# Kernel tuning notes

Measured on AMD Instinct MI355X. Metric: run time of the kernel, lower is better.

Reference implementation:

```python
import jax, jax.numpy as jnp
import numpy as np

N_NODES = 50000
N_EDGES = 500000
NODE_DIM = 128
EDGE_DIM = 64
OUT_DIM = 128


def setup_inputs() -> dict:
    key = jax.random.key(0)
    k1, k2, k3, k4, k5, k6 = jax.random.split(key, 6)
    node_feats = jax.random.normal(k1, (N_NODES, NODE_DIM), dtype=jnp.float32)
    edge_feats = jax.random.normal(k2, (N_EDGES, EDGE_DIM), dtype=jnp.float32)
    src_idx = jax.random.randint(k3, (N_EDGES,), 0, N_NODES, dtype=jnp.int32)
    dst_idx = jax.random.randint(k4, (N_EDGES,), 0, N_NODES, dtype=jnp.int32)
    in_dim = 2 * NODE_DIM + EDGE_DIM
    # nn.Linear-style init scale
    scale = 1.0 / np.sqrt(in_dim)
    W = jax.random.normal(k5, (in_dim, OUT_DIM), dtype=jnp.float32) * scale
    b = jax.random.normal(k6, (OUT_DIM,), dtype=jnp.float32) * scale
    return {"node_feats": node_feats, "edge_feats": edge_feats,
            "src_idx": src_idx, "dst_idx": dst_idx, "W": W, "b": b}


def reference(node_feats, edge_feats, src_idx, dst_idx, W, b):
    # Gather per-edge src/dst node features, concat with edge feats (residual=True)
    src = node_feats[src_idx]            # [E, node_dim]
    dst = node_feats[dst_idx]            # [E, node_dim]
    combined = jnp.concatenate([src, dst, edge_feats], axis=-1)  # [E, 2*nd+ed]
    score = combined @ W + b             # [E, out_dim]
    return score
```

## Files before the change

### kernel.cpp

```cpp
#include <hip/hip_runtime.h>
#include <hip/hip_bf16.h>
#include <cstdint>

#define N_NODES 50000
#define N_EDGES 500000
#define ND 128
#define ED 64
#define OD 128

typedef __attribute__((ext_vector_type(8))) short short8;
typedef __attribute__((ext_vector_type(4))) float f32x4;

__device__ __forceinline__ unsigned short f2bf(float f) {
    union { float f; unsigned u; } c; c.f = f;
    unsigned u = c.u;
    unsigned r = (u + 0x7FFFu + ((u >> 16) & 1u)) >> 16;
    return (unsigned short)r;
}
__device__ __forceinline__ float bf2f(unsigned short s) {
    union { unsigned u; float f; } c; c.u = ((unsigned)s) << 16;
    return c.f;
}

__global__ void prep_kernel(const float* __restrict__ W,
                            unsigned short* __restrict__ wbtNP,
                            unsigned short* __restrict__ wbtE) {
    int g = blockIdx.x * 256 + threadIdx.x;
    if (g < 256 * 128) {
        int n = g >> 7, k = g & 127;
        float v = (n < 128) ? W[k * OD + n] : W[(128 + k) * OD + (n - 128)];
        wbtNP[n * 128 + k] = f2bf(v);
    } else {
        int h = g - 256 * 128;
        int n = h >> 6, k = h & 63;
        wbtE[n * 64 + k] = f2bf(W[(256 + k) * OD + n]);
    }
}

__launch_bounds__(512)
__global__ void nodeproj_kernel(const float* __restrict__ nf,
                                const unsigned short* __restrict__ wbtNP,
                                unsigned short* __restrict__ P) {
    __shared__ char lds[16384 + 65536];
    int tid = threadIdx.x;
    int m0 = blockIdx.x * 64;

    for (int i = 0; i < 4; ++i) {
        int idx = tid + i * 512;
        int row = idx >> 5, c4 = idx & 31;
        int m = m0 + row;
        float4 v = make_float4(0.f, 0.f, 0.f, 0.f);
        if (m < N_NODES) v = *(const float4*)(nf + m * ND + c4 * 4);
        uint2 pk;
        pk.x = (unsigned)f2bf(v.x) | ((unsigned)f2bf(v.y) << 16);
        pk.y = (unsigned)f2bf(v.z) | ((unsigned)f2bf(v.w) << 16);
        int byte = (row * 256 + c4 * 8) ^ ((row & 7) << 4);
        *(uint2*)(lds + byte) = pk;
    }
    {
        const uint2* wsrc = (const uint2*)wbtNP;
        for (int i = 0; i < 16; ++i) {
            int idx = tid + i * 512;
            int row = idx >> 5, c4 = idx & 31;
            uint2 v = wsrc[row * 32 + c4];
            int byte = 16384 + ((row * 256 + c4 * 8) ^ ((row & 7) << 4));
            *(uint2*)(lds + byte) = v;
        }
    }
    __syncthreads();

    int lane = tid & 63, wid = tid >> 6;
    int wm = wid >> 1;
    int wn = wid & 1;
    f32x4 acc[8];
#pragma unroll
    for (int i = 0; i < 8; ++i) acc[i] = (f32x4){0.f, 0.f, 0.f, 0.f};

    int arow = 16 * wm + (lane & 15);
    int abase = arow * 256;
    int aswz = (arow & 7) << 4;
#pragma unroll
    for (int kc = 0; kc < 4; ++kc) {
        int kb = kc * 64 + ((lane >> 4) << 4);
        short8 a = *(const short8*)(lds + ((abase + kb) ^ aswz));
#pragma unroll
        for (int nt = 0; nt < 8; ++nt) {
            int brow = 128 * wn + 16 * nt + (lane & 15);
            short8 b = *(const short8*)(lds + 16384 + ((brow * 256 + kb) ^ ((brow & 7) << 4)));
            acc[nt] = __builtin_amdgcn_mfma_f32_16x16x32_bf16(a, b, acc[nt], 0, 0, 0);
        }
    }

    int mbase = m0 + 16 * wm + ((lane >> 4) << 2);
    int colbase = 128 * wn + (lane & 15);
#pragma unroll
    for (int nt = 0; nt < 8; ++nt) {
#pragma unroll
        for (int r = 0; r < 4; ++r) {
            int mm = mbase + r;
            if (mm < N_NODES) P[mm * 256 + colbase + 16 * nt] = f2bf(acc[nt][r]);
        }
    }
}

__launch_bounds__(256)
__global__ void edge_kernel(const float* __restrict__ ef,
                            const int* __restrict__ src,
                            const int* __restrict__ dst,
                            const unsigned short* __restrict__ wbtE,
                            const unsigned short* __restrict__ P,
                            const float* __restrict__ bias,
                            float* __restrict__ out) {
    __shared__ char lds[8192 + 16384 + 32768];
    int tid = threadIdx.x;
    int e0 = blockIdx.x * 64;

    for (int i = 0; i < 4; ++i) {
        int idx = tid + i * 256;
        int row = idx >> 4, c4 = idx & 15;
        int e = e0 + row;
        float4 v = make_float4(0.f, 0.f, 0.f, 0.f);
        if (e < N_EDGES) v = *(const float4*)(ef + e * ED + c4 * 4);
        uint2 pk;
        pk.x = (unsigned)f2bf(v.x) | ((unsigned)f2bf(v.y) << 16);
        pk.y = (unsigned)f2bf(v.z) | ((unsigned)f2bf(v.w) << 16);
        int byte = (row * 128 + c4 * 8) ^ ((row & 7) << 4);
        *(uint2*)(lds + byte) = pk;
    }
    {
        const uint2* wsrc = (const uint2*)wbtE;
        for (int i = 0; i < 8; ++i) {
            int idx = tid + i * 256;
            int row = idx >> 4, c4 = idx & 15;
            uint2 v = wsrc[row * 16 + c4];
            int byte = 8192 + ((row * 128 + c4 * 8) ^ ((row & 7) << 4));
            *(uint2*)(lds + byte) = v;
        }
    }
    __syncthreads();

    int lane = tid & 63, wid = tid >> 6;
    f32x4 acc[8];
#pragma unroll
    for (int i = 0; i < 8; ++i) acc[i] = (f32x4){0.f, 0.f, 0.f, 0.f};

    int arow = 16 * wid + (lane & 15);
#pragma unroll
    for (int kc = 0; kc < 2; ++kc) {
        int kb = kc * 64 + ((lane >> 4) << 4);
        short8 a = *(const short8*)(lds + ((arow * 128 + kb) ^ ((arow & 7) << 4)));
#pragma unroll
        for (int nt = 0; nt < 8; ++nt) {
            int brow = 16 * nt + (lane & 15);
            short8 b = *(const short8*)(lds + 8192 + ((brow * 128 + kb) ^ ((brow & 7) << 4)));
            acc[nt] = __builtin_amdgcn_mfma_f32_16x16x32_bf16(a, b, acc[nt], 0, 0, 0);
        }
    }

    {
        int rbase = 16 * wid + ((lane >> 4) << 2);
        int col = lane & 15;
#pragma unroll
        for (int nt = 0; nt < 8; ++nt) {
#pragma unroll
            for (int r = 0; r < 4; ++r) {
                int row = rbase + r;
                int cbyte = (col + 16 * nt) * 4;
                int byte = 24576 + ((row * 512 + cbyte) ^ (((row >> 2) & 3) << 4));
                *(float*)(lds + byte) = acc[nt][r];
            }
        }
    }
    __syncthreads();

    int l32 = tid & 31;
    float4 bv = *(const float4*)(bias + l32 * 4);
    const char* Pb = (const char*)P;
#pragma unroll
    for (int it = 0; it < 8; ++it) {
        int row = (tid >> 5) + it * 8;
        int e = e0 + row;
        if (e < N_EDGES) {
            float4 cb = *(const float4*)(lds + 24576 + ((row * 512 + l32 * 16) ^ (((row >> 2) & 3) << 4)));
            int s = src[e], d = dst[e];
            uint2 p1 = *(const uint2*)(Pb + s * 512 + l32 * 8);
            uint2 p2 = *(const uint2*)(Pb + d * 512 + 256 + l32 * 8);
            float4 o;
            o.x = cb.x + bv.x + bf2f((unsigned short)(p1.x & 0xFFFF)) + bf2f((unsigned short)(p2.x & 0xFFFF));
            o.y = cb.y + bv.y + bf2f((unsigned short)(p1.x >> 16))   + bf2f((unsigned short)(p2.x >> 16));
            o.z = cb.z + bv.z + bf2f((unsigned short)(p1.y & 0xFFFF)) + bf2f((unsigned short)(p2.y & 0xFFFF));
            o.w = cb.w + bv.w + bf2f((unsigned short)(p1.y >> 16))   + bf2f((unsigned short)(p2.y >> 16));
            *(float4*)(out + e * OD + l32 * 4) = o;
        }
    }
}

__global__ void naive_kernel(const float* __restrict__ nf, const float* __restrict__ ef,
                             const int* __restrict__ src, const int* __restrict__ dst,
                             const float* __restrict__ W, const float* __restrict__ bias,
                             float* __restrict__ out) {
    long g = (long)blockIdx.x * 256 + threadIdx.x;
    if (g >= (long)N_EDGES * OD) return;
    int e = (int)(g >> 7), j = (int)(g & 127);
    int s = src[e], d = dst[e];
    float sum = bias[j];
    for (int k = 0; k < ND; ++k) sum += nf[s * ND + k] * W[k * OD + j];
    for (int k = 0; k < ND; ++k) sum += nf[d * ND + k] * W[(ND + k) * OD + j];
    for (int k = 0; k < ED; ++k) sum += ef[e * ED + k] * W[(2 * ND + k) * OD + j];
    out[g] = sum;
}

extern "C" void kernel_launch(void* const* d_in, const int* in_sizes, int n_in,
                              void* d_out, int out_size, void* d_ws, size_t ws_size,
                              hipStream_t stream) {
    const float* nf  = (const float*)d_in[0];
    const float* ef  = (const float*)d_in[1];
    const int*   src = (const int*)d_in[2];
    const int*   dst = (const int*)d_in[3];
    const float* W   = (const float*)d_in[4];
    const float* bias= (const float*)d_in[5];
    float* out = (float*)d_out;

    const size_t need = 65536 + 16384 + (size_t)N_NODES * 256 * 2;
    if (ws_size < need) {
        long total = (long)N_EDGES * OD;
        naive_kernel<<<(int)((total + 255) / 256), 256, 0, stream>>>(nf, ef, src, dst, W, bias, out);
        return;
    }
    unsigned short* wbtNP = (unsigned short*)d_ws;
    unsigned short* wbtE  = (unsigned short*)((char*)d_ws + 65536);
    unsigned short* P     = (unsigned short*)((char*)d_ws + 81920);

    prep_kernel<<<160, 256, 0, stream>>>(W, wbtNP, wbtE);
    nodeproj_kernel<<<(N_NODES + 63) / 64, 512, 0, stream>>>(nf, wbtNP, P);
    edge_kernel<<<(N_EDGES + 63) / 64, 256, 0, stream>>>(ef, src, dst, wbtE, P, bias, out);
}
```

Baseline: 487.8 us.

## Swap MFMA operands so accumulators map to rows, drop LDS epilogue staging

Both GEMMs now pass the weight tile as the A operand and the activations as B. Each lane's accumulators then hold four consecutive output columns of one row, so results are written straight from registers. This removes the edge kernel's 32KB LDS staging buffer and its second barrier, and the gathered node-projection rows are read and added directly into the accumulators. Node projection stores and weight loads become packed 64-bit agent-scope atomic operations, and nodeproj runs with 256 threads per block, each wave covering all 256 output columns. The cost is more accumulator registers per thread in nodeproj, and the relaxed atomics may restrict how the compiler handles those loads and stores.

```diff
diff --git a/kernel.cpp b/kernel.cpp
--- a/kernel.cpp
+++ b/kernel.cpp
@@ -10,6 +10,7 @@
 
 typedef __attribute__((ext_vector_type(8))) short short8;
 typedef __attribute__((ext_vector_type(4))) float f32x4;
+typedef unsigned long long u64;
 
 __device__ __forceinline__ unsigned short f2bf(float f) {
     union { float f; unsigned u; } c; c.f = f;
@@ -22,31 +23,51 @@
     return c.f;
 }
 
+__device__ __forceinline__ void store_u64_agent(u64* p, u64 v) {
+    __hip_atomic_store(p, v, __ATOMIC_RELAXED, __HIP_MEMORY_SCOPE_AGENT);
+}
+__device__ __forceinline__ u64 load_u64_agent(const u64* p) {
+    return __hip_atomic_load(const_cast<u64*>(p), __ATOMIC_RELAXED, __HIP_MEMORY_SCOPE_AGENT);
+}
+
 __global__ void prep_kernel(const float* __restrict__ W,
-                            unsigned short* __restrict__ wbtNP,
-                            unsigned short* __restrict__ wbtE) {
+                            u64* __restrict__ wbtNP64,
+                            u64* __restrict__ wbtE64) {
     int g = blockIdx.x * 256 + threadIdx.x;
-    if (g < 256 * 128) {
-        int n = g >> 7, k = g & 127;
-        float v = (n < 128) ? W[k * OD + n] : W[(128 + k) * OD + (n - 128)];
-        wbtNP[n * 128 + k] = f2bf(v);
-    } else {
-        int h = g - 256 * 128;
-        int n = h >> 6, k = h & 63;
-        wbtE[n * 64 + k] = f2bf(W[(256 + k) * OD + n]);
-    }
-}
-
-__launch_bounds__(512)
+    if (g < 8192) {
+        int n = g >> 5, k0 = (g & 31) * 4;
+        u64 v = 0;
+#pragma unroll
+        for (int j = 0; j < 4; ++j) {
+            int k = k0 + j;
+            float f = (n < 128) ? W[k * OD + n] : W[(128 + k) * OD + (n - 128)];
+            v |= ((u64)f2bf(f)) << (16 * j);
+        }
+        store_u64_agent(wbtNP64 + g, v);
+    } else if (g < 10240) {
+        int h = g - 8192;
+        int n = h >> 4, k0 = (h & 15) * 4;
+        u64 v = 0;
+#pragma unroll
+        for (int j = 0; j < 4; ++j) {
+            int k = k0 + j;
+            v |= ((u64)f2bf(W[(256 + k) * OD + n])) << (16 * j);
+        }
+        store_u64_agent(wbtE64 + h, v);
+    }
+}
+
+__launch_bounds__(256)
 __global__ void nodeproj_kernel(const float* __restrict__ nf,
-                                const unsigned short* __restrict__ wbtNP,
-                                unsigned short* __restrict__ P) {
+                                const u64* __restrict__ wbtNP64,
+                                u64* __restrict__ P64) {
     __shared__ char lds[16384 + 65536];
     int tid = threadIdx.x;
     int m0 = blockIdx.x * 64;
 
-    for (int i = 0; i < 4; ++i) {
-        int idx = tid + i * 512;
+#pragma unroll
+    for (int i = 0; i < 8; ++i) {
+        int idx = tid + i * 256;
         int row = idx >> 5, c4 = idx & 31;
         int m = m0 + row;
         float4 v = make_float4(0.f, 0.f, 0.f, 0.f);
@@ -57,48 +78,45 @@
         int byte = (row * 256 + c4 * 8) ^ ((row & 7) << 4);
         *(uint2*)(lds + byte) = pk;
     }
-    {
-        const uint2* wsrc = (const uint2*)wbtNP;
-        for (int i = 0; i < 16; ++i) {
-            int idx = tid + i * 512;
-            int row = idx >> 5, c4 = idx & 31;
-            uint2 v = wsrc[row * 32 + c4];
-            int byte = 16384 + ((row * 256 + c4 * 8) ^ ((row & 7) << 4));
-            *(uint2*)(lds + byte) = v;
-        }
+#pragma unroll
+    for (int i = 0; i < 32; ++i) {
+        int idx = tid + i * 256;
+        int row = idx >> 5, c4 = idx & 31;
+        u64 v = load_u64_agent(wbtNP64 + row * 32 + c4);
+        int byte = 16384 + ((row * 256 + c4 * 8) ^ ((row & 7) << 4));
+        *(u64*)(lds + byte) = v;
     }
     __syncthreads();
 
     int lane = tid & 63, wid = tid >> 6;
-    int wm = wid >> 1;
-    int wn = wid & 1;
-    f32x4 acc[8];
-#pragma unroll
-    for (int i = 0; i < 8; ++i) acc[i] = (f32x4){0.f, 0.f, 0.f, 0.f};
-
-    int arow = 16 * wm + (lane & 15);
-    int abase = arow * 256;
-    int aswz = (arow & 7) << 4;
+    f32x4 acc[16];
+#pragma unroll
+    for (int i = 0; i < 16; ++i) acc[i] = (f32x4){0.f, 0.f, 0.f, 0.f};
+
+    int mrow = 16 * wid + (lane & 15);
+    int abase = mrow * 256;
+    int aswz = (mrow & 7) << 4;
 #pragma unroll
     for (int kc = 0; kc < 4; ++kc) {
         int kb = kc * 64 + ((lane >> 4) << 4);
-        short8 a = *(const short8*)(lds + ((abase + kb) ^ aswz));
-#pragma unroll
-        for (int nt = 0; nt < 8; ++nt) {
-            int brow = 128 * wn + 16 * nt + (lane & 15);
-            short8 b = *(const short8*)(lds + 16384 + ((brow * 256 + kb) ^ ((brow & 7) << 4)));
-            acc[nt] = __builtin_amdgcn_mfma_f32_16x16x32_bf16(a, b, acc[nt], 0, 0, 0);
-        }
-    }
-
-    int mbase = m0 + 16 * wm + ((lane >> 4) << 2);
-    int colbase = 128 * wn + (lane & 15);
-#pragma unroll
-    for (int nt = 0; nt < 8; ++nt) {
-#pragma unroll
-        for (int r = 0; r < 4; ++r) {
-            int mm = mbase + r;
-            if (mm < N_NODES) P[mm * 256 + colbase + 16 * nt] = f2bf(acc[nt][r]);
+        short8 nfr = *(const short8*)(lds + ((abase + kb) ^ aswz));
+#pragma unroll
+        for (int mt = 0; mt < 16; ++mt) {
+            int n = 16 * mt + (lane & 15);
+            short8 w = *(const short8*)(lds + 16384 + ((n * 256 + kb) ^ ((n & 7) << 4)));
+            acc[mt] = __builtin_amdgcn_mfma_f32_16x16x32_bf16(w, nfr, acc[mt], 0, 0, 0);
+        }
+    }
+
+    int m = m0 + mrow;
+    if (m < N_NODES) {
+        int lg = lane >> 4;
+        u64* Prow = P64 + (size_t)m * 64;
+#pragma unroll
+        for (int mt = 0; mt < 16; ++mt) {
+            unsigned lo = (unsigned)f2bf(acc[mt][0]) | ((unsigned)f2bf(acc[mt][1]) << 16);
+            unsigned hi = (unsigned)f2bf(acc[mt][2]) | ((unsigned)f2bf(acc[mt][3]) << 16);
+            store_u64_agent(Prow + mt * 4 + lg, (u64)lo | ((u64)hi << 32));
         }
     }
 }
@@ -107,14 +125,15 @@
 __global__ void edge_kernel(const float* __restrict__ ef,
                             const int* __restrict__ src,
                             const int* __restrict__ dst,
-                            const unsigned short* __restrict__ wbtE,
-                            const unsigned short* __restrict__ P,
+                            const u64* __restrict__ wbtE64,
+                            const u64* __restrict__ P64,
                             const float* __restrict__ bias,
                             float* __restrict__ out) {
-    __shared__ char lds[8192 + 16384 + 32768];
+    __shared__ char lds[8192 + 16384];
     int tid = threadIdx.x;
     int e0 = blockIdx.x * 64;
 
+#pragma unroll
     for (int i = 0; i < 4; ++i) {
         int idx = tid + i * 256;
         int row = idx >> 4, c4 = idx & 15;
@@ -127,71 +146,60 @@
         int byte = (row * 128 + c4 * 8) ^ ((row & 7) << 4);
         *(uint2*)(lds + byte) = pk;
     }
-    {
-        const uint2* wsrc = (const uint2*)wbtE;
-        for (int i = 0; i < 8; ++i) {
-            int idx = tid + i * 256;
-            int row = idx >> 4, c4 = idx & 15;
-            uint2 v = wsrc[row * 16 + c4];
-            int byte = 8192 + ((row * 128 + c4 * 8) ^ ((row & 7) << 4));
-            *(uint2*)(lds + byte) = v;
-        }
+#pragma unroll
+    for (int i = 0; i < 8; ++i) {
+        int idx = tid + i * 256;
+        int row = idx >> 4, c4 = idx & 15;
+        u64 v = load_u64_agent(wbtE64 + row * 16 + c4);
+        int byte = 8192 + ((row * 128 + c4 * 8) ^ ((row & 7) << 4));
+        *(u64*)(lds + byte) = v;
     }
     __syncthreads();
 
-    int lane = tid & 63, wid = tid >> 6;
+    int lane = tid & 63, wid = tid >> 6, lg = lane >> 4;
     f32x4 acc[8];
 #pragma unroll
     for (int i = 0; i < 8; ++i) acc[i] = (f32x4){0.f, 0.f, 0.f, 0.f};
 
-    int arow = 16 * wid + (lane & 15);
+    int erow = 16 * wid + (lane & 15);
+    int ebase = erow * 128;
+    int eswz = (erow & 7) << 4;
 #pragma unroll
     for (int kc = 0; kc < 2; ++kc) {
-        int kb = kc * 64 + ((lane >> 4) << 4);
-        short8 a = *(const short8*)(lds + ((arow * 128 + kb) ^ ((arow & 7) << 4)));
-#pragma unroll
-        for (int nt = 0; nt < 8; ++nt) {
-            int brow = 16 * nt + (lane & 15);
-            short8 b = *(const short8*)(lds + 8192 + ((brow * 128 + kb) ^ ((brow & 7) << 4)));
-            acc[nt] = __builtin_amdgcn_mfma_f32_16x16x32_bf16(a, b, acc[nt], 0, 0, 0);
-        }
-    }
-
-    {
-        int rbase = 16 * wid + ((lane >> 4) << 2);
-        int col = lane & 15;
-#pragma unroll
-        for (int nt = 0; nt < 8; ++nt) {
-#pragma unroll
-            for (int r = 0; r < 4; ++r) {
-                int row = rbase + r;
-                int cbyte = (col + 16 * nt) * 4;
-                int byte = 24576 + ((row * 512 + cbyte) ^ (((row >> 2) & 3) << 4));
-                *(float*)(lds + byte) = acc[nt][r];
-            }
-        }
-    }
-    __syncthreads();
-
-    int l32 = tid & 31;
-    float4 bv = *(const float4*)(bias + l32 * 4);
-    const char* Pb = (const char*)P;
-#pragma unroll
-    for (int it = 0; it < 8; ++it) {
-        int row = (tid >> 5) + it * 8;
-        int e = e0 + row;
-        if (e < N_EDGES) {
-            float4 cb = *(const float4*)(lds + 24576 + ((row * 512 + l32 * 16) ^ (((row >> 2) & 3) << 4)));
-            int s = src[e], d = dst[e];
-            uint2 p1 = *(const uint2*)(Pb + s * 512 + l32 * 8);
-            uint2 p2 = *(const uint2*)(Pb + d * 512 + 256 + l32 * 8);
-            float4 o;
-            o.x = cb.x + bv.x + bf2f((unsigned short)(p1.x & 0xFFFF)) + bf2f((unsigned short)(p2.x & 0xFFFF));
-            o.y = cb.y + bv.y + bf2f((unsigned short)(p1.x >> 16))   + bf2f((unsigned short)(p2.x >> 16));
-            o.z = cb.z + bv.z + bf2f((unsigned short)(p1.y & 0xFFFF)) + bf2f((unsigned short)(p2.y & 0xFFFF));
-            o.w = cb.w + bv.w + bf2f((unsigned short)(p1.y >> 16))   + bf2f((unsigned short)(p2.y >> 16));
-            *(float4*)(out + e * OD + l32 * 4) = o;
-        }
+        int kb = kc * 64 + (lg << 4);
+        short8 efr = *(const short8*)(lds + ((ebase + kb) ^ eswz));
+#pragma unroll
+        for (int mt = 0; mt < 8; ++mt) {
+            int n = 16 * mt + (lane & 15);
+            short8 w = *(const short8*)(lds + 8192 + ((n * 128 + kb) ^ ((n & 7) << 4)));
+            acc[mt] = __builtin_amdgcn_mfma_f32_16x16x32_bf16(w, efr, acc[mt], 0, 0, 0);
+        }
+    }
+
+    int e = e0 + erow;
+    bool ok = e < N_EDGES;
+    int ec = ok ? e : (N_EDGES - 1);
+    int s = src[ec], d = dst[ec];
+    const u64* Ps = P64 + (size_t)s * 64;
+    const u64* Pd = P64 + (size_t)d * 64 + 32;
+    u64 g1[8], g2[8];
+#pragma unroll
+    for (int mt = 0; mt < 8; ++mt) {
+        g1[mt] = load_u64_agent(Ps + mt * 4 + lg);
+        g2[mt] = load_u64_agent(Pd + mt * 4 + lg);
+    }
+    float* orow = out + (size_t)e * OD + 4 * lg;
+#pragma unroll
+    for (int mt = 0; mt < 8; ++mt) {
+        float4 bv = *(const float4*)(bias + 16 * mt + 4 * lg);
+        unsigned p1x = (unsigned)g1[mt], p1y = (unsigned)(g1[mt] >> 32);
+        unsigned p2x = (unsigned)g2[mt], p2y = (unsigned)(g2[mt] >> 32);
+        float4 o;
+        o.x = acc[mt][0] + bv.x + bf2f((unsigned short)(p1x & 0xFFFF)) + bf2f((unsigned short)(p2x & 0xFFFF));
+        o.y = acc[mt][1] + bv.y + bf2f((unsigned short)(p1x >> 16))    + bf2f((unsigned short)(p2x >> 16));
+        o.z = acc[mt][2] + bv.z + bf2f((unsigned short)(p1y & 0xFFFF)) + bf2f((unsigned short)(p2y & 0xFFFF));
+        o.w = acc[mt][3] + bv.w + bf2f((unsigned short)(p1y >> 16))    + bf2f((unsigned short)(p2y >> 16));
+        if (ok) *(float4*)(orow + 16 * mt) = o;
     }
 }
 
@@ -221,17 +229,17 @@
     const float* bias= (const float*)d_in[5];
     float* out = (float*)d_out;
 
-    const size_t need = 65536 + 16384 + (size_t)N_NODES * 256 * 2;
+    const size_t need = 65536 + 16384 + (size_t)N_NODES * 512;
     if (ws_size < need) {
         long total = (long)N_EDGES * OD;
         naive_kernel<<<(int)((total + 255) / 256), 256, 0, stream>>>(nf, ef, src, dst, W, bias, out);
         return;
     }
-    unsigned short* wbtNP = (unsigned short*)d_ws;
-    unsigned short* wbtE  = (unsigned short*)((char*)d_ws + 65536);
-    unsigned short* P     = (unsigned short*)((char*)d_ws + 81920);
-
-    prep_kernel<<<160, 256, 0, stream>>>(W, wbtNP, wbtE);
-    nodeproj_kernel<<<(N_NODES + 63) / 64, 512, 0, stream>>>(nf, wbtNP, P);
-    edge_kernel<<<(N_EDGES + 63) / 64, 256, 0, stream>>>(ef, src, dst, wbtE, P, bias, out);
-}
+    u64* wbtNP64 = (u64*)d_ws;
+    u64* wbtE64  = (u64*)((char*)d_ws + 65536);
+    u64* P64     = (u64*)((char*)d_ws + 81920);
+
+    prep_kernel<<<40, 256, 0, stream>>>(W, wbtNP64, wbtE64);
+    nodeproj_kernel<<<(N_NODES + 63) / 64, 256, 0, stream>>>(nf, wbtNP64, P64);
+    edge_kernel<<<(N_EDGES + 63) / 64, 256, 0, stream>>>(ef, src, dst, wbtE64, P64, bias, out);
+}
```

After: 495.7 us. Within noise of the previous version (+1.6%).
